# Performance work log

Hardware: AMD Instinct MI355X
Metric: run time of the kernel (lower is better)

The kernel has to match this reference:

```python
import jax, jax.numpy as jnp
import numpy as np

N = 50000          # nodes
E = 800000         # edges
F_IN, H, OUT = 512, 256, 2
BN_EPS = 1e-5


def setup_inputs() -> dict:
    key = jax.random.key(0)
    ks = jax.random.split(key, 10)
    x = jax.random.normal(ks[0], (N, F_IN), jnp.float32)
    edge_index = jax.random.randint(ks[1], (2, E), 0, N, dtype=jnp.int64)
    edge_weight = jax.random.uniform(ks[2], (E,), jnp.float32)

    def lin(k, fan_in, fan_out):
        return jax.random.normal(k, (fan_in, fan_out), jnp.float32) / np.sqrt(fan_in).astype(np.float32)

    W1, b1 = lin(ks[3], F_IN, H), jnp.zeros((H,), jnp.float32)
    W2, b2 = lin(ks[4], H, H), jnp.zeros((H,), jnp.float32)
    W3, b3 = lin(ks[5], H, OUT), jnp.zeros((OUT,), jnp.float32)
    # BatchNorm1d affine params + running stats (eval mode)
    g1, be1 = jnp.ones((H,), jnp.float32), jnp.zeros((H,), jnp.float32)
    m1 = 0.1 * jax.random.normal(ks[6], (H,), jnp.float32)
    v1 = jax.random.uniform(ks[7], (H,), jnp.float32, 0.5, 1.5)
    g2, be2 = jnp.ones((H,), jnp.float32), jnp.zeros((H,), jnp.float32)
    m2 = 0.1 * jax.random.normal(ks[8], (H,), jnp.float32)
    v2 = jax.random.uniform(ks[9], (H,), jnp.float32, 0.5, 1.5)
    return {"x": x, "edge_index": edge_index, "edge_weight": edge_weight,
            "W1": W1, "b1": b1, "g1": g1, "be1": be1, "m1": m1, "v1": v1,
            "W2": W2, "b2": b2, "g2": g2, "be2": be2, "m2": m2, "v2": v2,
            "W3": W3, "b3": b3}


def gcn_conv(x, row, col, w, W, b):
    # PyG GCNConv (eval): h = x @ W; out[col] += norm * h[row]; + b
    # row/col/w already include self-loops with weight 1.
    n = x.shape[0]
    h = x @ W                                      # [N, out]
    deg = jax.ops.segment_sum(w, col, num_segments=n)
    dinv = jnp.where(deg > 0, jax.lax.rsqrt(deg), 0.0)
    norm = dinv[row] * w * dinv[col]               # [E+N]
    out = jax.ops.segment_sum(h[row] * norm[:, None], col, num_segments=n)
    return out + b


def batchnorm_eval(x, g, be, m, v):
    return (x - m) * jax.lax.rsqrt(v + BN_EPS) * g + be


def reference(x, edge_index, edge_weight, W1, b1, g1, be1, m1, v1,
              W2, b2, g2, be2, m2, v2, W3, b3):
    n = x.shape[0]
    loops = jnp.arange(n, dtype=edge_index.dtype)
    row = jnp.concatenate([edge_index[0], loops])
    col = jnp.concatenate([edge_index[1], loops])
    w = jnp.concatenate([edge_weight, jnp.ones((n,), x.dtype)])

    h = jax.nn.relu(batchnorm_eval(gcn_conv(x, row, col, w, W1, b1), g1, be1, m1, v1))
    h = jax.nn.relu(batchnorm_eval(gcn_conv(h, row, col, w, W2, b2), g2, be2, m2, v2))
    return gcn_conv(h, row, col, w, W3, b3)
```

## Files before the change

kernel.cpp:

```cpp
#include <hip/hip_runtime.h>
#include <stdint.h>

#define F_IN 512
#define HF 256
#define OUT_F 2
#define BN_EPS 1e-5f
#define SCAN_B 256
#define LDSTR 36

typedef __attribute__((ext_vector_type(8))) short bf16x8;
typedef __attribute__((ext_vector_type(8))) unsigned short u16x8;
typedef __attribute__((ext_vector_type(4))) float f32x4;

__device__ inline float bf2f(unsigned short u) {
    union { float f; uint32_t i; } v; v.i = ((uint32_t)u) << 16; return v.f;
}
__device__ inline unsigned short f2bf(float f) {
    union { float f; uint32_t i; } v; v.f = f;
    uint32_t r = v.i + 0x7FFFu + ((v.i >> 16) & 1u);
    return (unsigned short)(r >> 16);
}

__global__ void prep_kernel(unsigned long long* __restrict__ packed,
                            const float* __restrict__ W1, unsigned short* __restrict__ W1t,
                            const float* __restrict__ W2, unsigned short* __restrict__ W2t,
                            unsigned short* __restrict__ xbf_pad,
                            unsigned short* __restrict__ bufa_pad,
                            int n, int padx, int pada) {
    int idx = blockIdx.x * blockDim.x + threadIdx.x;
    if (idx < n) { packed[idx] = 1ULL << 20; return; }
    int j = idx - n;
    if (j < F_IN * HF) {
        int nn = j >> 9, k = j & (F_IN - 1);
        W1t[j] = f2bf(W1[(size_t)k * HF + nn]);
        return;
    }
    j -= F_IN * HF;
    if (j < HF * HF) {
        int nn = j >> 8, k = j & (HF - 1);
        W2t[j] = f2bf(W2[(size_t)k * HF + nn]);
        return;
    }
    j -= HF * HF;
    if (j < padx) { xbf_pad[j] = 0; return; }
    j -= padx;
    if (j < pada) bufa_pad[j] = 0;
}

__global__ void count_conv_kernel(const int* __restrict__ col,
                                  const float* __restrict__ w,
                                  unsigned long long* __restrict__ packed,
                                  const float* __restrict__ x,
                                  unsigned short* __restrict__ xbf,
                                  int e, int nchunk) {
    int tid = blockIdx.x * blockDim.x + threadIdx.x;
    if (tid < e) {
        unsigned long long add = (1ULL << 40)
            | (unsigned long long)__float2uint_rn(w[tid] * 1048576.0f);
        atomicAdd(&packed[col[tid]], add);
    }
    const int stride = gridDim.x * blockDim.x;
    const float4* x4 = (const float4*)x;
    for (int c = tid; c < nchunk; c += stride) {
        float4 f0 = x4[2 * c];
        float4 f1 = x4[2 * c + 1];
        bf16x8 v;
        v[0] = (short)f2bf(f0.x); v[1] = (short)f2bf(f0.y);
        v[2] = (short)f2bf(f0.z); v[3] = (short)f2bf(f0.w);
        v[4] = (short)f2bf(f1.x); v[5] = (short)f2bf(f1.y);
        v[6] = (short)f2bf(f1.z); v[7] = (short)f2bf(f1.w);
        *(bf16x8*)(xbf + (size_t)c * 8) = v;
    }
}

__global__ __launch_bounds__(256)
void gemm_kernel(const unsigned short* __restrict__ A,
                 const unsigned short* __restrict__ Bt,
                 unsigned short* __restrict__ C, int K) {
    __shared__ unsigned short As[2][128 * LDSTR];
    __shared__ unsigned short Bs[2][128 * LDSTR];
    const int tid  = threadIdx.x;
    const int lane = tid & 63;
    const int wv   = tid >> 6;
    const int wrow = wv >> 1, wcol = wv & 1;
    const int m0 = blockIdx.x * 128;
    const int n0 = blockIdx.y * 128;

    const int sr = tid >> 2;
    const int sc = (tid & 3) * 8;

    const unsigned short* pa0 = A + (size_t)(m0 + sr) * K + sc;
    const unsigned short* pa1 = A + (size_t)(m0 + sr + 64) * K + sc;
    const unsigned short* pb0 = Bt + (size_t)(n0 + sr) * K + sc;
    const unsigned short* pb1 = Bt + (size_t)(n0 + sr + 64) * K + sc;

    f32x4 zero4 = {0.0f, 0.0f, 0.0f, 0.0f};
    f32x4 acc[4][4];
    #pragma unroll
    for (int i = 0; i < 4; ++i)
        #pragma unroll
        for (int j = 0; j < 4; ++j) acc[i][j] = zero4;

    const int q8 = (lane >> 4) * 8;
    const int ml = lane & 15;

    bf16x8 va0 = *(const bf16x8*)pa0;
    bf16x8 va1 = *(const bf16x8*)pa1;
    bf16x8 vb0 = *(const bf16x8*)pb0;
    bf16x8 vb1 = *(const bf16x8*)pb1;

    const int nsteps = K >> 5;
    for (int s = 0; s < nsteps; ++s) {
        const int buf = s & 1;
        *(bf16x8*)&As[buf][sr * LDSTR + sc]        = va0;
        *(bf16x8*)&As[buf][(sr + 64) * LDSTR + sc] = va1;
        *(bf16x8*)&Bs[buf][sr * LDSTR + sc]        = vb0;
        *(bf16x8*)&Bs[buf][(sr + 64) * LDSTR + sc] = vb1;
        __syncthreads();
        if (s + 1 < nsteps) {
            int off = (s + 1) * 32;
            va0 = *(const bf16x8*)(pa0 + off);
            va1 = *(const bf16x8*)(pa1 + off);
            vb0 = *(const bf16x8*)(pb0 + off);
            vb1 = *(const bf16x8*)(pb1 + off);
        }
        bf16x8 af[4], bfr[4];
        #pragma unroll
        for (int i = 0; i < 4; ++i)
            af[i] = *(const bf16x8*)&As[buf][(wrow * 64 + i * 16 + ml) * LDSTR + q8];
        #pragma unroll
        for (int j = 0; j < 4; ++j)
            bfr[j] = *(const bf16x8*)&Bs[buf][(wcol * 64 + j * 16 + ml) * LDSTR + q8];
        #pragma unroll
        for (int i = 0; i < 4; ++i)
            #pragma unroll
            for (int j = 0; j < 4; ++j)
                acc[i][j] = __builtin_amdgcn_mfma_f32_16x16x32_bf16(af[i], bfr[j], acc[i][j], 0, 0, 0);
    }

    const int q4 = (lane >> 4) * 4;
    #pragma unroll
    for (int i = 0; i < 4; ++i) {
        #pragma unroll
        for (int j = 0; j < 4; ++j) {
            #pragma unroll
            for (int rg = 0; rg < 4; ++rg) {
                int r = m0 + wrow * 64 + i * 16 + q4 + rg;
                int c = n0 + wcol * 64 + j * 16 + ml;
                C[(size_t)r * HF + c] = f2bf(acc[i][j][rg]);
            }
        }
    }
}

__global__ void scan1_kernel(const unsigned long long* __restrict__ packed,
                             int* __restrict__ local, int* __restrict__ blocksum, int n) {
    __shared__ int tmp[SCAN_B];
    int i = blockIdx.x * SCAN_B + threadIdx.x;
    int v = (i < n) ? (int)(packed[i] >> 40) : 0;
    tmp[threadIdx.x] = v;
    __syncthreads();
    for (int off = 1; off < SCAN_B; off <<= 1) {
        int t = 0;
        if ((int)threadIdx.x >= off) t = tmp[threadIdx.x - off];
        __syncthreads();
        if ((int)threadIdx.x >= off) tmp[threadIdx.x] += t;
        __syncthreads();
    }
    if (i < n) local[i] = tmp[threadIdx.x] - v;
    if (threadIdx.x == SCAN_B - 1) blocksum[blockIdx.x] = tmp[SCAN_B - 1];
}

__global__ void scan3_dinv_kernel(int* __restrict__ csr_ptr, int* __restrict__ cursor,
                                  const int* __restrict__ blocksum,
                                  const unsigned long long* __restrict__ packed,
                                  float* __restrict__ dinv, int n, int e, int nb) {
    __shared__ int red[SCAN_B];
    int t = threadIdx.x;
    red[t] = (t < nb && t < (int)blockIdx.x) ? blocksum[t] : 0;
    __syncthreads();
    for (int off = SCAN_B / 2; off > 0; off >>= 1) {
        if (t < off) red[t] += red[t + off];
        __syncthreads();
    }
    int prefix = red[0];
    int i = blockIdx.x * SCAN_B + t;
    if (i < n) {
        int val = csr_ptr[i] + prefix;
        csr_ptr[i] = val;
        cursor[i] = val;
        float deg = (float)(packed[i] & 0xFFFFFFFFFFULL) * (1.0f / 1048576.0f);
        dinv[i] = rsqrtf(deg);
    }
    if (i == 0) csr_ptr[n] = e;
}

__global__ void fill_kernel(const int* __restrict__ row, const int* __restrict__ col,
                            const float* __restrict__ w, const float* __restrict__ dinv,
                            int* __restrict__ cursor, int2* __restrict__ csr_edge, int e) {
    int i = blockIdx.x * blockDim.x + threadIdx.x;
    if (i < e) {
        int r = row[i], c = col[i];
        int pos = atomicAdd(&cursor[c], 1);
        float nrm = dinv[r] * w[i] * dinv[c];
        csr_edge[pos] = make_int2(r, __float_as_int(nrm));
    }
}

#define AGBL 8
template<int FINAL>
__global__ void agg_kernel(const unsigned short* __restrict__ h,
                           const int* __restrict__ ptr,
                           const int2* __restrict__ edge,
                           const float* __restrict__ dinv,
                           const float* __restrict__ b, const float* __restrict__ g,
                           const float* __restrict__ be, const float* __restrict__ m,
                           const float* __restrict__ v,
                           unsigned short* __restrict__ out,
                           const float* __restrict__ W3, float* __restrict__ h3, int n) {
    int wid  = (blockIdx.x * blockDim.x + threadIdx.x) >> 6;
    int lane = threadIdx.x & 63;
    if (wid >= n) return;
    const int hi = lane >> 5;
    const int l  = lane & 31;
    const int fo = l * 8;

    int p0 = ptr[wid], p1 = ptr[wid + 1];
    int deg = p1 - p0;

    float a0 = 0.f, a1 = 0.f, a2 = 0.f, a3 = 0.f;
    float a4 = 0.f, a5 = 0.f, a6 = 0.f, a7 = 0.f;

    const int nb = deg & ~15;
    for (int t = 0; t < nb; t += 16) {
        int2 ed[AGBL];
        #pragma unroll
        for (int k = 0; k < AGBL; ++k) ed[k] = edge[p0 + t + 2 * k + hi];
        u16x8 hv[AGBL];
        #pragma unroll
        for (int k = 0; k < AGBL; ++k)
            hv[k] = *(const u16x8*)(h + (size_t)(unsigned)ed[k].x * HF + fo);
        #pragma unroll
        for (int k = 0; k < AGBL; ++k) {
            float nw = __int_as_float(ed[k].y);
            a0 += nw * bf2f(hv[k][0]);
            a1 += nw * bf2f(hv[k][1]);
            a2 += nw * bf2f(hv[k][2]);
            a3 += nw * bf2f(hv[k][3]);
            a4 += nw * bf2f(hv[k][4]);
            a5 += nw * bf2f(hv[k][5]);
            a6 += nw * bf2f(hv[k][6]);
            a7 += nw * bf2f(hv[k][7]);
        }
    }
    for (int t = nb; t < deg; t += 4) {
        int2 ed[2];
        float wv2[2];
        #pragma unroll
        for (int j = 0; j < 2; ++j) {
            int idx = t + 2 * j + hi;
            int cl = idx < deg ? idx : 0;
            ed[j] = edge[p0 + cl];
            wv2[j] = (idx < deg) ? __int_as_float(ed[j].y) : 0.0f;
        }
        u16x8 hv[2];
        #pragma unroll
        for (int j = 0; j < 2; ++j)
            hv[j] = *(const u16x8*)(h + (size_t)(unsigned)ed[j].x * HF + fo);
        #pragma unroll
        for (int j = 0; j < 2; ++j) {
            float nw = wv2[j];
            a0 += nw * bf2f(hv[j][0]);
            a1 += nw * bf2f(hv[j][1]);
            a2 += nw * bf2f(hv[j][2]);
            a3 += nw * bf2f(hv[j][3]);
            a4 += nw * bf2f(hv[j][4]);
            a5 += nw * bf2f(hv[j][5]);
            a6 += nw * bf2f(hv[j][6]);
            a7 += nw * bf2f(hv[j][7]);
        }
    }

    a0 += __shfl_xor(a0, 32, 64);
    a1 += __shfl_xor(a1, 32, 64);
    a2 += __shfl_xor(a2, 32, 64);
    a3 += __shfl_xor(a3, 32, 64);
    a4 += __shfl_xor(a4, 32, 64);
    a5 += __shfl_xor(a5, 32, 64);
    a6 += __shfl_xor(a6, 32, 64);
    a7 += __shfl_xor(a7, 32, 64);

    float s = dinv[wid];
    float sl = s * s;
    u16x8 hs = *(const u16x8*)(h + (size_t)wid * HF + fo);
    a0 += sl * bf2f(hs[0]);
    a1 += sl * bf2f(hs[1]);
    a2 += sl * bf2f(hs[2]);
    a3 += sl * bf2f(hs[3]);
    a4 += sl * bf2f(hs[4]);
    a5 += sl * bf2f(hs[5]);
    a6 += sl * bf2f(hs[6]);
    a7 += sl * bf2f(hs[7]);

    float4 bb0  = *(const float4*)(b + fo),      bb1  = *(const float4*)(b + fo + 4);
    float4 gg0  = *(const float4*)(g + fo),      gg1  = *(const float4*)(g + fo + 4);
    float4 bee0 = *(const float4*)(be + fo),     bee1 = *(const float4*)(be + fo + 4);
    float4 mm0  = *(const float4*)(m + fo),      mm1  = *(const float4*)(m + fo + 4);
    float4 vv0  = *(const float4*)(v + fo),      vv1  = *(const float4*)(v + fo + 4);
    float f0 = fmaxf((a0 + bb0.x - mm0.x) * rsqrtf(vv0.x + BN_EPS) * gg0.x + bee0.x, 0.f);
    float f1 = fmaxf((a1 + bb0.y - mm0.y) * rsqrtf(vv0.y + BN_EPS) * gg0.y + bee0.y, 0.f);
    float f2 = fmaxf((a2 + bb0.z - mm0.z) * rsqrtf(vv0.z + BN_EPS) * gg0.z + bee0.z, 0.f);
    float f3 = fmaxf((a3 + bb0.w - mm0.w) * rsqrtf(vv0.w + BN_EPS) * gg0.w + bee0.w, 0.f);
    float f4 = fmaxf((a4 + bb1.x - mm1.x) * rsqrtf(vv1.x + BN_EPS) * gg1.x + bee1.x, 0.f);
    float f5 = fmaxf((a5 + bb1.y - mm1.y) * rsqrtf(vv1.y + BN_EPS) * gg1.y + bee1.y, 0.f);
    float f6 = fmaxf((a6 + bb1.z - mm1.z) * rsqrtf(vv1.z + BN_EPS) * gg1.z + bee1.z, 0.f);
    float f7 = fmaxf((a7 + bb1.w - mm1.w) * rsqrtf(vv1.w + BN_EPS) * gg1.w + bee1.w, 0.f);

    if (!FINAL) {
        if (hi == 0) {
            u16x8 o;
            o[0] = f2bf(f0); o[1] = f2bf(f1); o[2] = f2bf(f2); o[3] = f2bf(f3);
            o[4] = f2bf(f4); o[5] = f2bf(f5); o[6] = f2bf(f6); o[7] = f2bf(f7);
            *(u16x8*)(out + (size_t)wid * HF + fo) = o;
        }
    } else {
        float4 w0 = *(const float4*)(W3 + fo * 2);
        float4 w1 = *(const float4*)(W3 + fo * 2 + 4);
        float4 w2 = *(const float4*)(W3 + fo * 2 + 8);
        float4 w3 = *(const float4*)(W3 + fo * 2 + 12);
        float s0 = f0 * w0.x + f1 * w0.z + f2 * w1.x + f3 * w1.z
                 + f4 * w2.x + f5 * w2.z + f6 * w3.x + f7 * w3.z;
        float s1 = f0 * w0.y + f1 * w0.w + f2 * w1.y + f3 * w1.w
                 + f4 * w2.y + f5 * w2.w + f6 * w3.y + f7 * w3.w;
        #pragma unroll
        for (int o = 16; o > 0; o >>= 1) {
            s0 += __shfl_xor(s0, o, 64);
            s1 += __shfl_xor(s1, o, 64);
        }
        if (lane == 0) {
            h3[wid * 2 + 0] = s0;
            h3[wid * 2 + 1] = s1;
        }
    }
}

__global__ void out_kernel(const float* __restrict__ h3,
                           const int* __restrict__ ptr, const int2* __restrict__ edge,
                           const float* __restrict__ dinv,
                           const float* __restrict__ b3, float* __restrict__ out, int n) {
    int i = blockIdx.x * blockDim.x + threadIdx.x;
    if (i >= n) return;
    int p0 = ptr[i], p1 = ptr[i + 1];
    float a0 = 0.f, a1 = 0.f;
    for (int p = p0; p < p1; p += 4) {
        #pragma unroll
        for (int k = 0; k < 4; ++k) {
            int idx = p + k < p1 ? p + k : p1 - 1;
            int2 e = edge[idx];
            float nw = (p + k < p1) ? __int_as_float(e.y) : 0.0f;
            float2 u = *(const float2*)(h3 + 2 * e.x);
            a0 += nw * u.x;
            a1 += nw * u.y;
        }
    }
    float s = dinv[i];
    float sl = s * s;
    out[2 * i + 0] = a0 + sl * h3[2 * i + 0] + b3[0];
    out[2 * i + 1] = a1 + sl * h3[2 * i + 1] + b3[1];
}

static inline char* align16(char* p) {
    return (char*)(((uintptr_t)p + 15) & ~(uintptr_t)15);
}

extern "C" void kernel_launch(void* const* d_in, const int* in_sizes, int n_in,
                              void* d_out, int out_size, void* d_ws, size_t ws_size,
                              hipStream_t stream) {
    const float* x   = (const float*)d_in[0];
    const int*   ei  = (const int*)d_in[1];
    const float* ew  = (const float*)d_in[2];
    const float* W1  = (const float*)d_in[3];
    const float* b1  = (const float*)d_in[4];
    const float* g1  = (const float*)d_in[5];
    const float* be1 = (const float*)d_in[6];
    const float* m1  = (const float*)d_in[7];
    const float* v1  = (const float*)d_in[8];
    const float* W2  = (const float*)d_in[9];
    const float* b2  = (const float*)d_in[10];
    const float* g2  = (const float*)d_in[11];
    const float* be2 = (const float*)d_in[12];
    const float* m2  = (const float*)d_in[13];
    const float* v2  = (const float*)d_in[14];
    const float* W3  = (const float*)d_in[15];
    const float* b3  = (const float*)d_in[16];

    const int N  = in_sizes[0] / F_IN;
    const int E  = in_sizes[2];
    const int MP = (N + 127) & ~127;
    const int* row = ei;
    const int* col = ei + E;

    char* wsb = (char*)d_ws;
    unsigned long long* packed = (unsigned long long*)wsb; wsb = align16(wsb + (size_t)N * 8);
    float* dinv     = (float*)wsb;          wsb = align16(wsb + (size_t)N * 4);
    int*   csr_ptr  = (int*)wsb;            wsb = align16(wsb + (size_t)(N + 1) * 4);
    int*   cursor   = (int*)wsb;            wsb = align16(wsb + (size_t)N * 4);
    int*   blocksum = (int*)wsb;            wsb = align16(wsb + (size_t)SCAN_B * 4);
    int2*  csr_edge = (int2*)wsb;           wsb = align16(wsb + (size_t)E * 8);
    unsigned short* W1t = (unsigned short*)wsb;  wsb = align16(wsb + (size_t)F_IN * HF * 2);
    unsigned short* W2t = (unsigned short*)wsb;  wsb = align16(wsb + (size_t)HF * HF * 2);
    unsigned short* xbf  = (unsigned short*)wsb; wsb = align16(wsb + (size_t)MP * F_IN * 2);
    unsigned short* bufh = (unsigned short*)wsb; wsb = align16(wsb + (size_t)MP * HF * 2);
    unsigned short* bufa = (unsigned short*)wsb; wsb = align16(wsb + (size_t)MP * HF * 2);
    float* h3 = (float*)wsb;                wsb = align16(wsb + (size_t)N * OUT_F * 4);
    float* outf = (float*)d_out;

    const int TB = 256;
    const int nscan = (N + SCAN_B - 1) / SCAN_B;
    const int padx = (MP - N) * F_IN;
    const int pada = (MP - N) * HF;
    const int preptot = N + F_IN * HF + HF * HF + padx + pada;
    const int ncc = (E + TB - 1) / TB;
    const int nchunk = (N * F_IN) / 8;

    prep_kernel<<<(preptot + TB - 1) / TB, TB, 0, stream>>>(
        packed, W1, W1t, W2, W2t, xbf + (size_t)N * F_IN, bufa + (size_t)N * HF, N, padx, pada);

    count_conv_kernel<<<ncc, TB, 0, stream>>>(col, ew, packed, x, xbf, E, nchunk);

    scan1_kernel<<<nscan, SCAN_B, 0, stream>>>(packed, csr_ptr, blocksum, N);
    scan3_dinv_kernel<<<nscan, SCAN_B, 0, stream>>>(csr_ptr, cursor, blocksum, packed, dinv, N, E, nscan);
    fill_kernel<<<(E + TB - 1) / TB, TB, 0, stream>>>(row, col, ew, dinv, cursor, csr_edge, E);

    dim3 ggrid(MP / 128, HF / 128);

    gemm_kernel<<<ggrid, TB, 0, stream>>>(xbf, W1t, bufh, F_IN);
    agg_kernel<0><<<((size_t)N * 64 + TB - 1) / TB, TB, 0, stream>>>(
        bufh, csr_ptr, csr_edge, dinv, b1, g1, be1, m1, v1, bufa, nullptr, nullptr, N);

    gemm_kernel<<<ggrid, TB, 0, stream>>>(bufa, W2t, bufh, HF);
    agg_kernel<1><<<((size_t)N * 64 + TB - 1) / TB, TB, 0, stream>>>(
        bufh, csr_ptr, csr_edge, dinv, b2, g2, be2, m2, v2, nullptr, W3, h3, N);

    out_kernel<<<(N + TB - 1) / TB, TB, 0, stream>>>(h3, csr_ptr, csr_edge, dinv, b3, outf, N);
}
```

Baseline: 467.1 us.

## Fuse fp32-to-bf16 input conversion into first GEMM and prefetch edges in aggregation

The first GEMM now reads the fp32 node features directly and converts them to bf16 while loading its A tile, clamping out-of-range rows instead of relying on a zero-padded bf16 copy. This drops the separate conversion pass that wrote a bf16 copy of x, along with its workspace and padding fill. Because the GEMM grid has two column blocks, each fp32 row is read twice and converted twice, so the GEMM does more memory traffic and ALU work. Separately, the aggregation kernel's main loop prefetches the next batch of CSR edge entries before accumulating the current one, to hide the latency of the dependent gather.

```diff
diff --git a/kernel.cpp b/kernel.cpp
--- a/kernel.cpp
+++ b/kernel.cpp
@@ -24,9 +24,8 @@
 __global__ void prep_kernel(unsigned long long* __restrict__ packed,
                             const float* __restrict__ W1, unsigned short* __restrict__ W1t,
                             const float* __restrict__ W2, unsigned short* __restrict__ W2t,
-                            unsigned short* __restrict__ xbf_pad,
                             unsigned short* __restrict__ bufa_pad,
-                            int n, int padx, int pada) {
+                            int n, int pada) {
     int idx = blockIdx.x * blockDim.x + threadIdx.x;
     if (idx < n) { packed[idx] = 1ULL << 20; return; }
     int j = idx - n;
@@ -42,41 +41,42 @@
         return;
     }
     j -= HF * HF;
-    if (j < padx) { xbf_pad[j] = 0; return; }
-    j -= padx;
     if (j < pada) bufa_pad[j] = 0;
 }
 
-__global__ void count_conv_kernel(const int* __restrict__ col,
-                                  const float* __restrict__ w,
-                                  unsigned long long* __restrict__ packed,
-                                  const float* __restrict__ x,
-                                  unsigned short* __restrict__ xbf,
-                                  int e, int nchunk) {
+__global__ void count_kernel(const int* __restrict__ col,
+                             const float* __restrict__ w,
+                             unsigned long long* __restrict__ packed, int e) {
     int tid = blockIdx.x * blockDim.x + threadIdx.x;
     if (tid < e) {
         unsigned long long add = (1ULL << 40)
             | (unsigned long long)__float2uint_rn(w[tid] * 1048576.0f);
         atomicAdd(&packed[col[tid]], add);
     }
-    const int stride = gridDim.x * blockDim.x;
-    const float4* x4 = (const float4*)x;
-    for (int c = tid; c < nchunk; c += stride) {
-        float4 f0 = x4[2 * c];
-        float4 f1 = x4[2 * c + 1];
-        bf16x8 v;
-        v[0] = (short)f2bf(f0.x); v[1] = (short)f2bf(f0.y);
-        v[2] = (short)f2bf(f0.z); v[3] = (short)f2bf(f0.w);
-        v[4] = (short)f2bf(f1.x); v[5] = (short)f2bf(f1.y);
-        v[6] = (short)f2bf(f1.z); v[7] = (short)f2bf(f1.w);
-        *(bf16x8*)(xbf + (size_t)c * 8) = v;
-    }
-}
-
+}
+
+template<int AFP32>
+__device__ inline bf16x8 load_a(const void* base, size_t elem_off) {
+    if constexpr (AFP32) {
+        const float* p = (const float*)base + elem_off;
+        float4 f0 = *(const float4*)p;
+        float4 f1 = *(const float4*)(p + 4);
+        bf16x8 r;
+        r[0] = (short)f2bf(f0.x); r[1] = (short)f2bf(f0.y);
+        r[2] = (short)f2bf(f0.z); r[3] = (short)f2bf(f0.w);
+        r[4] = (short)f2bf(f1.x); r[5] = (short)f2bf(f1.y);
+        r[6] = (short)f2bf(f1.z); r[7] = (short)f2bf(f1.w);
+        return r;
+    } else {
+        return *(const bf16x8*)((const unsigned short*)base + elem_off);
+    }
+}
+
+template<int AFP32>
 __global__ __launch_bounds__(256)
-void gemm_kernel(const unsigned short* __restrict__ A,
+void gemm_kernel(const void* __restrict__ Av,
                  const unsigned short* __restrict__ Bt,
-                 unsigned short* __restrict__ C, int K) {
+                 unsigned short* __restrict__ C, int K, int rowclamp) {
     __shared__ unsigned short As[2][128 * LDSTR];
     __shared__ unsigned short Bs[2][128 * LDSTR];
     const int tid  = threadIdx.x;
@@ -89,8 +89,14 @@
     const int sr = tid >> 2;
     const int sc = (tid & 3) * 8;
 
-    const unsigned short* pa0 = A + (size_t)(m0 + sr) * K + sc;
-    const unsigned short* pa1 = A + (size_t)(m0 + sr + 64) * K + sc;
+    int ra0 = m0 + sr, ra1 = m0 + sr + 64;
+    if (AFP32) {
+        ra0 = ra0 < rowclamp ? ra0 : rowclamp - 1;
+        ra1 = ra1 < rowclamp ? ra1 : rowclamp - 1;
+    }
+    const size_t offA0 = (size_t)ra0 * K + sc;
+    const size_t offA1 = (size_t)ra1 * K + sc;
+
     const unsigned short* pb0 = Bt + (size_t)(n0 + sr) * K + sc;
     const unsigned short* pb1 = Bt + (size_t)(n0 + sr + 64) * K + sc;
 
@@ -104,8 +110,8 @@
     const int q8 = (lane >> 4) * 8;
     const int ml = lane & 15;
 
-    bf16x8 va0 = *(const bf16x8*)pa0;
-    bf16x8 va1 = *(const bf16x8*)pa1;
+    bf16x8 va0 = load_a<AFP32>(Av, offA0);
+    bf16x8 va1 = load_a<AFP32>(Av, offA1);
     bf16x8 vb0 = *(const bf16x8*)pb0;
     bf16x8 vb1 = *(const bf16x8*)pb1;
 
@@ -119,8 +125,8 @@
         __syncthreads();
         if (s + 1 < nsteps) {
             int off = (s + 1) * 32;
-            va0 = *(const bf16x8*)(pa0 + off);
-            va1 = *(const bf16x8*)(pa1 + off);
+            va0 = load_a<AFP32>(Av, offA0 + off);
+            va1 = load_a<AFP32>(Av, offA1 + off);
             vb0 = *(const bf16x8*)(pb0 + off);
             vb1 = *(const bf16x8*)(pb1 + off);
         }
@@ -232,25 +238,33 @@
     float a4 = 0.f, a5 = 0.f, a6 = 0.f, a7 = 0.f;
 
     const int nb = deg & ~15;
-    for (int t = 0; t < nb; t += 16) {
-        int2 ed[AGBL];
-        #pragma unroll
-        for (int k = 0; k < AGBL; ++k) ed[k] = edge[p0 + t + 2 * k + hi];
-        u16x8 hv[AGBL];
-        #pragma unroll
-        for (int k = 0; k < AGBL; ++k)
-            hv[k] = *(const u16x8*)(h + (size_t)(unsigned)ed[k].x * HF + fo);
-        #pragma unroll
-        for (int k = 0; k < AGBL; ++k) {
-            float nw = __int_as_float(ed[k].y);
-            a0 += nw * bf2f(hv[k][0]);
-            a1 += nw * bf2f(hv[k][1]);
-            a2 += nw * bf2f(hv[k][2]);
-            a3 += nw * bf2f(hv[k][3]);
-            a4 += nw * bf2f(hv[k][4]);
-            a5 += nw * bf2f(hv[k][5]);
-            a6 += nw * bf2f(hv[k][6]);
-            a7 += nw * bf2f(hv[k][7]);
+    if (nb > 0) {
+        int2 edc[AGBL];
+        #pragma unroll
+        for (int k = 0; k < AGBL; ++k) edc[k] = edge[p0 + 2 * k + hi];
+        for (int t = 0; t < nb; t += 16) {
+            u16x8 hv[AGBL];
+            #pragma unroll
+            for (int k = 0; k < AGBL; ++k)
+                hv[k] = *(const u16x8*)(h + (size_t)(unsigned)edc[k].x * HF + fo);
+            float wv[AGBL];
+            #pragma unroll
+            for (int k = 0; k < AGBL; ++k) wv[k] = __int_as_float(edc[k].y);
+            if (t + 16 < nb) {
+                #pragma unroll
+                for (int k = 0; k < AGBL; ++k) edc[k] = edge[p0 + t + 16 + 2 * k + hi];
+            }
+            #pragma unroll
+            for (int k = 0; k < AGBL; ++k) {
+                a0 += wv[k] * bf2f(hv[k][0]);
+                a1 += wv[k] * bf2f(hv[k][1]);
+                a2 += wv[k] * bf2f(hv[k][2]);
+                a3 += wv[k] * bf2f(hv[k][3]);
+                a4 += wv[k] * bf2f(hv[k][4]);
+                a5 += wv[k] * bf2f(hv[k][5]);
+                a6 += wv[k] * bf2f(hv[k][6]);
+                a7 += wv[k] * bf2f(hv[k][7]);
+            }
         }
     }
     for (int t = nb; t < deg; t += 4) {
@@ -409,7 +423,6 @@
     int2*  csr_edge = (int2*)wsb;           wsb = align16(wsb + (size_t)E * 8);
     unsigned short* W1t = (unsigned short*)wsb;  wsb = align16(wsb + (size_t)F_IN * HF * 2);
     unsigned short* W2t = (unsigned short*)wsb;  wsb = align16(wsb + (size_t)HF * HF * 2);
-    unsigned short* xbf  = (unsigned short*)wsb; wsb = align16(wsb + (size_t)MP * F_IN * 2);
     unsigned short* bufh = (unsigned short*)wsb; wsb = align16(wsb + (size_t)MP * HF * 2);
     unsigned short* bufa = (unsigned short*)wsb; wsb = align16(wsb + (size_t)MP * HF * 2);
     float* h3 = (float*)wsb;                wsb = align16(wsb + (size_t)N * OUT_F * 4);
@@ -417,16 +430,13 @@
 
     const int TB = 256;
     const int nscan = (N + SCAN_B - 1) / SCAN_B;
-    const int padx = (MP - N) * F_IN;
     const int pada = (MP - N) * HF;
-    const int preptot = N + F_IN * HF + HF * HF + padx + pada;
-    const int ncc = (E + TB - 1) / TB;
-    const int nchunk = (N * F_IN) / 8;
+    const int preptot = N + F_IN * HF + HF * HF + pada;
 
     prep_kernel<<<(preptot + TB - 1) / TB, TB, 0, stream>>>(
-        packed, W1, W1t, W2, W2t, xbf + (size_t)N * F_IN, bufa + (size_t)N * HF, N, padx, pada);
-
-    count_conv_kernel<<<ncc, TB, 0, stream>>>(col, ew, packed, x, xbf, E, nchunk);
+        packed, W1, W1t, W2, W2t, bufa + (size_t)N * HF, N, pada);
+
+    count_kernel<<<(E + TB - 1) / TB, TB, 0, stream>>>(col, ew, packed, E);
 
     scan1_kernel<<<nscan, SCAN_B, 0, stream>>>(packed, csr_ptr, blocksum, N);
     scan3_dinv_kernel<<<nscan, SCAN_B, 0, stream>>>(csr_ptr, cursor, blocksum, packed, dinv, N, E, nscan);
@@ -434,11 +444,11 @@
 
     dim3 ggrid(MP / 128, HF / 128);
 
-    gemm_kernel<<<ggrid, TB, 0, stream>>>(xbf, W1t, bufh, F_IN);
+    gemm_kernel<1><<<ggrid, TB, 0, stream>>>(x, W1t, bufh, F_IN, N);
     agg_kernel<0><<<((size_t)N * 64 + TB - 1) / TB, TB, 0, stream>>>(
         bufh, csr_ptr, csr_edge, dinv, b1, g1, be1, m1, v1, bufa, nullptr, nullptr, N);
 
-    gemm_kernel<<<ggrid, TB, 0, stream>>>(bufa, W2t, bufh, HF);
+    gemm_kernel<0><<<ggrid, TB, 0, stream>>>(bufa, W2t, bufh, HF, MP);
     agg_kernel<1><<<((size_t)N * 64 + TB - 1) / TB, TB, 0, stream>>>(
         bufh, csr_ptr, csr_edge, dinv, b2, g2, be2, m2, v2, nullptr, W3, h3, N);
 
```

Measured after the change: 476.6 us. +2.0%, slower.

## Fuse graph setup kernels into one persistent kernel with grid barriers

Applied to the files above, without the earlier changes.

Merges the prep, count/convert, two scan and fill kernels into a single persistent setup kernel of 768 blocks that separates phases with a software grid-wide barrier built on atomics. This removes four kernel launches and the gaps between them in the preprocessing pipeline. It adds a memset of the barrier counters, relies on all 768 blocks being co-resident (launch bounds 256,4 on 256 CUs) to avoid deadlock, and the atomic spin barriers cost time of their own.

```diff
diff --git a/kernel.cpp b/kernel.cpp
--- a/kernel.cpp
+++ b/kernel.cpp
@@ -7,6 +7,7 @@
 #define BN_EPS 1e-5f
 #define SCAN_B 256
 #define LDSTR 36
+#define NBSETUP 768
 
 typedef __attribute__((ext_vector_type(8))) short bf16x8;
 typedef __attribute__((ext_vector_type(8))) unsigned short u16x8;
@@ -21,47 +22,56 @@
     return (unsigned short)(r >> 16);
 }
 
-__global__ void prep_kernel(unsigned long long* __restrict__ packed,
-                            const float* __restrict__ W1, unsigned short* __restrict__ W1t,
-                            const float* __restrict__ W2, unsigned short* __restrict__ W2t,
-                            unsigned short* __restrict__ xbf_pad,
-                            unsigned short* __restrict__ bufa_pad,
-                            int n, int padx, int pada) {
-    int idx = blockIdx.x * blockDim.x + threadIdx.x;
-    if (idx < n) { packed[idx] = 1ULL << 20; return; }
-    int j = idx - n;
-    if (j < F_IN * HF) {
+__device__ inline void grid_sync(int* cnt, int* gen, int nb) {
+    __syncthreads();
+    if (threadIdx.x == 0) {
+        __threadfence();
+        int g = __hip_atomic_load(gen, __ATOMIC_RELAXED, __HIP_MEMORY_SCOPE_AGENT);
+        if (__hip_atomic_fetch_add(cnt, 1, __ATOMIC_ACQ_REL, __HIP_MEMORY_SCOPE_AGENT) == nb - 1) {
+            __hip_atomic_store(cnt, 0, __ATOMIC_RELAXED, __HIP_MEMORY_SCOPE_AGENT);
+            __hip_atomic_store(gen, g + 1, __ATOMIC_RELEASE, __HIP_MEMORY_SCOPE_AGENT);
+        } else {
+            while (__hip_atomic_load(gen, __ATOMIC_ACQUIRE, __HIP_MEMORY_SCOPE_AGENT) == g)
+                __builtin_amdgcn_s_sleep(2);
+        }
+        __threadfence();
+    }
+    __syncthreads();
+}
+
+__global__ __launch_bounds__(256, 4)
+void setup_kernel(unsigned long long* __restrict__ packed,
+                  const float* __restrict__ W1, unsigned short* __restrict__ W1t,
+                  const float* __restrict__ W2, unsigned short* __restrict__ W2t,
+                  unsigned short* __restrict__ xbf,
+                  unsigned short* __restrict__ bufa,
+                  const float* __restrict__ x,
+                  const int* __restrict__ row, const int* __restrict__ col,
+                  const float* __restrict__ ew,
+                  int* __restrict__ csr_ptr, int* __restrict__ cursor,
+                  int* __restrict__ blocksum, float* __restrict__ dinv,
+                  int2* __restrict__ csr_edge,
+                  int* __restrict__ bar,
+                  int n, int e, int padx, int pada, int nscan, int nchunk) {
+    __shared__ int tmp[SCAN_B];
+    const int gsz  = gridDim.x * blockDim.x;
+    const int gtid = blockIdx.x * blockDim.x + threadIdx.x;
+    int* cnt = bar;
+    int* gen = bar + 1;
+
+    for (int i = gtid; i < n; i += gsz) packed[i] = 1ULL << 20;
+    for (int j = gtid; j < F_IN * HF; j += gsz) {
         int nn = j >> 9, k = j & (F_IN - 1);
         W1t[j] = f2bf(W1[(size_t)k * HF + nn]);
-        return;
-    }
-    j -= F_IN * HF;
-    if (j < HF * HF) {
+    }
+    for (int j = gtid; j < HF * HF; j += gsz) {
         int nn = j >> 8, k = j & (HF - 1);
         W2t[j] = f2bf(W2[(size_t)k * HF + nn]);
-        return;
-    }
-    j -= HF * HF;
-    if (j < padx) { xbf_pad[j] = 0; return; }
-    j -= padx;
-    if (j < pada) bufa_pad[j] = 0;
-}
-
-__global__ void count_conv_kernel(const int* __restrict__ col,
-                                  const float* __restrict__ w,
-                                  unsigned long long* __restrict__ packed,
-                                  const float* __restrict__ x,
-                                  unsigned short* __restrict__ xbf,
-                                  int e, int nchunk) {
-    int tid = blockIdx.x * blockDim.x + threadIdx.x;
-    if (tid < e) {
-        unsigned long long add = (1ULL << 40)
-            | (unsigned long long)__float2uint_rn(w[tid] * 1048576.0f);
-        atomicAdd(&packed[col[tid]], add);
-    }
-    const int stride = gridDim.x * blockDim.x;
+    }
+    for (int j = gtid; j < padx; j += gsz) xbf[(size_t)n * F_IN + j] = 0;
+    for (int j = gtid; j < pada; j += gsz) bufa[(size_t)n * HF + j] = 0;
     const float4* x4 = (const float4*)x;
-    for (int c = tid; c < nchunk; c += stride) {
+    for (int c = gtid; c < nchunk; c += gsz) {
         float4 f0 = x4[2 * c];
         float4 f1 = x4[2 * c + 1];
         bf16x8 v;
@@ -70,6 +80,59 @@
         v[4] = (short)f2bf(f1.x); v[5] = (short)f2bf(f1.y);
         v[6] = (short)f2bf(f1.z); v[7] = (short)f2bf(f1.w);
         *(bf16x8*)(xbf + (size_t)c * 8) = v;
+    }
+    grid_sync(cnt, gen, (int)gridDim.x);
+
+    for (int i = gtid; i < e; i += gsz) {
+        unsigned long long add = (1ULL << 40)
+            | (unsigned long long)__float2uint_rn(ew[i] * 1048576.0f);
+        atomicAdd(&packed[col[i]], add);
+    }
+    grid_sync(cnt, gen, (int)gridDim.x);
+
+    if ((int)blockIdx.x < nscan) {
+        int i = blockIdx.x * SCAN_B + threadIdx.x;
+        int v = (i < n) ? (int)(packed[i] >> 40) : 0;
+        tmp[threadIdx.x] = v;
+        __syncthreads();
+        for (int off = 1; off < SCAN_B; off <<= 1) {
+            int t = 0;
+            if ((int)threadIdx.x >= off) t = tmp[threadIdx.x - off];
+            __syncthreads();
+            if ((int)threadIdx.x >= off) tmp[threadIdx.x] += t;
+            __syncthreads();
+        }
+        if (i < n) csr_ptr[i] = tmp[threadIdx.x] - v;
+        if (threadIdx.x == SCAN_B - 1) blocksum[blockIdx.x] = tmp[SCAN_B - 1];
+    }
+    grid_sync(cnt, gen, (int)gridDim.x);
+
+    if ((int)blockIdx.x < nscan) {
+        int t = threadIdx.x;
+        tmp[t] = (t < nscan && t < (int)blockIdx.x) ? blocksum[t] : 0;
+        __syncthreads();
+        for (int off = SCAN_B / 2; off > 0; off >>= 1) {
+            if (t < off) tmp[t] += tmp[t + off];
+            __syncthreads();
+        }
+        int prefix = tmp[0];
+        int i = blockIdx.x * SCAN_B + t;
+        if (i < n) {
+            int val = csr_ptr[i] + prefix;
+            csr_ptr[i] = val;
+            cursor[i] = val;
+            float deg = (float)(packed[i] & 0xFFFFFFFFFFULL) * (1.0f / 1048576.0f);
+            dinv[i] = rsqrtf(deg);
+        }
+        if (i == 0) csr_ptr[n] = e;
+    }
+    grid_sync(cnt, gen, (int)gridDim.x);
+
+    for (int i = gtid; i < e; i += gsz) {
+        int r = row[i], c = col[i];
+        int pos = atomicAdd(&cursor[c], 1);
+        float nrm = dinv[r] * ew[i] * dinv[c];
+        csr_edge[pos] = make_int2(r, __float_as_int(nrm));
     }
 }
 
@@ -150,60 +213,6 @@
                 C[(size_t)r * HF + c] = f2bf(acc[i][j][rg]);
             }
         }
-    }
-}
-
-__global__ void scan1_kernel(const unsigned long long* __restrict__ packed,
-                             int* __restrict__ local, int* __restrict__ blocksum, int n) {
-    __shared__ int tmp[SCAN_B];
-    int i = blockIdx.x * SCAN_B + threadIdx.x;
-    int v = (i < n) ? (int)(packed[i] >> 40) : 0;
-    tmp[threadIdx.x] = v;
-    __syncthreads();
-    for (int off = 1; off < SCAN_B; off <<= 1) {
-        int t = 0;
-        if ((int)threadIdx.x >= off) t = tmp[threadIdx.x - off];
-        __syncthreads();
-        if ((int)threadIdx.x >= off) tmp[threadIdx.x] += t;
-        __syncthreads();
-    }
-    if (i < n) local[i] = tmp[threadIdx.x] - v;
-    if (threadIdx.x == SCAN_B - 1) blocksum[blockIdx.x] = tmp[SCAN_B - 1];
-}
-
-__global__ void scan3_dinv_kernel(int* __restrict__ csr_ptr, int* __restrict__ cursor,
-                                  const int* __restrict__ blocksum,
-                                  const unsigned long long* __restrict__ packed,
-                                  float* __restrict__ dinv, int n, int e, int nb) {
-    __shared__ int red[SCAN_B];
-    int t = threadIdx.x;
-    red[t] = (t < nb && t < (int)blockIdx.x) ? blocksum[t] : 0;
-    __syncthreads();
-    for (int off = SCAN_B / 2; off > 0; off >>= 1) {
-        if (t < off) red[t] += red[t + off];
-        __syncthreads();
-    }
-    int prefix = red[0];
-    int i = blockIdx.x * SCAN_B + t;
-    if (i < n) {
-        int val = csr_ptr[i] + prefix;
-        csr_ptr[i] = val;
-        cursor[i] = val;
-        float deg = (float)(packed[i] & 0xFFFFFFFFFFULL) * (1.0f / 1048576.0f);
-        dinv[i] = rsqrtf(deg);
-    }
-    if (i == 0) csr_ptr[n] = e;
-}
-
-__global__ void fill_kernel(const int* __restrict__ row, const int* __restrict__ col,
-                            const float* __restrict__ w, const float* __restrict__ dinv,
-                            int* __restrict__ cursor, int2* __restrict__ csr_edge, int e) {
-    int i = blockIdx.x * blockDim.x + threadIdx.x;
-    if (i < e) {
-        int r = row[i], c = col[i];
-        int pos = atomicAdd(&cursor[c], 1);
-        float nrm = dinv[r] * w[i] * dinv[c];
-        csr_edge[pos] = make_int2(r, __float_as_int(nrm));
     }
 }
 
@@ -413,24 +422,21 @@
     unsigned short* bufh = (unsigned short*)wsb; wsb = align16(wsb + (size_t)MP * HF * 2);
     unsigned short* bufa = (unsigned short*)wsb; wsb = align16(wsb + (size_t)MP * HF * 2);
     float* h3 = (float*)wsb;                wsb = align16(wsb + (size_t)N * OUT_F * 4);
+    int*   bar = (int*)wsb;                 wsb = align16(wsb + 2 * 4);
     float* outf = (float*)d_out;
 
     const int TB = 256;
     const int nscan = (N + SCAN_B - 1) / SCAN_B;
     const int padx = (MP - N) * F_IN;
     const int pada = (MP - N) * HF;
-    const int preptot = N + F_IN * HF + HF * HF + padx + pada;
-    const int ncc = (E + TB - 1) / TB;
     const int nchunk = (N * F_IN) / 8;
 
-    prep_kernel<<<(preptot + TB - 1) / TB, TB, 0, stream>>>(
-        packed, W1, W1t, W2, W2t, xbf + (size_t)N * F_IN, bufa + (size_t)N * HF, N, padx, pada);
-
-    count_conv_kernel<<<ncc, TB, 0, stream>>>(col, ew, packed, x, xbf, E, nchunk);
-
-    scan1_kernel<<<nscan, SCAN_B, 0, stream>>>(packed, csr_ptr, blocksum, N);
-    scan3_dinv_kernel<<<nscan, SCAN_B, 0, stream>>>(csr_ptr, cursor, blocksum, packed, dinv, N, E, nscan);
-    fill_kernel<<<(E + TB - 1) / TB, TB, 0, stream>>>(row, col, ew, dinv, cursor, csr_edge, E);
+    (void)hipMemsetAsync(bar, 0, 2 * sizeof(int), stream);
+
+    setup_kernel<<<NBSETUP, TB, 0, stream>>>(
+        packed, W1, W1t, W2, W2t, xbf, bufa, x, row, col, ew,
+        csr_ptr, cursor, blocksum, dinv, csr_edge, bar,
+        N, E, padx, pada, nscan, nchunk);
 
     dim3 ggrid(MP / 128, HF / 128);
 
```

Result: slower. 922.3 us (+97.4%).

## Fuse prep kernels, co-launch CSR fill with first GEMM, add XCD swizzle

Applied to the files above, without the earlier changes.

Merges weight transpose, padding zeroing, degree counting and x-to-bf16 conversion into one grid-stride front kernel, and replaces the packed-init with a memset plus adding the self-loop degree in scan3. The CSR fill blocks are appended to the first GEMM launch so the atomic scatter overlaps with MFMA work. GEMM blocks are remapped with an XCD-aware swizzle so neighbouring tiles land on the same chiplet for L2 reuse. Together these cut launch count and idle tails, at the cost of heterogeneous blocks sharing LDS allocation and a fixed 1024-block front grid.

```diff
diff --git a/kernel.cpp b/kernel.cpp
--- a/kernel.cpp
+++ b/kernel.cpp
@@ -21,47 +21,33 @@
     return (unsigned short)(r >> 16);
 }
 
-__global__ void prep_kernel(unsigned long long* __restrict__ packed,
-                            const float* __restrict__ W1, unsigned short* __restrict__ W1t,
-                            const float* __restrict__ W2, unsigned short* __restrict__ W2t,
-                            unsigned short* __restrict__ xbf_pad,
-                            unsigned short* __restrict__ bufa_pad,
-                            int n, int padx, int pada) {
-    int idx = blockIdx.x * blockDim.x + threadIdx.x;
-    if (idx < n) { packed[idx] = 1ULL << 20; return; }
-    int j = idx - n;
-    if (j < F_IN * HF) {
+__global__ void front_kernel(unsigned long long* __restrict__ packed,
+                             const float* __restrict__ W1, unsigned short* __restrict__ W1t,
+                             const float* __restrict__ W2, unsigned short* __restrict__ W2t,
+                             const float* __restrict__ x, unsigned short* __restrict__ xbf,
+                             unsigned short* __restrict__ bufa_pad,
+                             const int* __restrict__ col, const float* __restrict__ ew,
+                             int n, int e, int padx, int pada, int nchunk) {
+    const int gsz  = gridDim.x * blockDim.x;
+    const int gtid = blockIdx.x * blockDim.x + threadIdx.x;
+
+    for (int i = gtid; i < e; i += gsz) {
+        unsigned long long add = (1ULL << 40)
+            | (unsigned long long)__float2uint_rn(ew[i] * 1048576.0f);
+        atomicAdd(&packed[col[i]], add);
+    }
+    for (int j = gtid; j < F_IN * HF; j += gsz) {
         int nn = j >> 9, k = j & (F_IN - 1);
         W1t[j] = f2bf(W1[(size_t)k * HF + nn]);
-        return;
-    }
-    j -= F_IN * HF;
-    if (j < HF * HF) {
+    }
+    for (int j = gtid; j < HF * HF; j += gsz) {
         int nn = j >> 8, k = j & (HF - 1);
         W2t[j] = f2bf(W2[(size_t)k * HF + nn]);
-        return;
-    }
-    j -= HF * HF;
-    if (j < padx) { xbf_pad[j] = 0; return; }
-    j -= padx;
-    if (j < pada) bufa_pad[j] = 0;
-}
-
-__global__ void count_conv_kernel(const int* __restrict__ col,
-                                  const float* __restrict__ w,
-                                  unsigned long long* __restrict__ packed,
-                                  const float* __restrict__ x,
-                                  unsigned short* __restrict__ xbf,
-                                  int e, int nchunk) {
-    int tid = blockIdx.x * blockDim.x + threadIdx.x;
-    if (tid < e) {
-        unsigned long long add = (1ULL << 40)
-            | (unsigned long long)__float2uint_rn(w[tid] * 1048576.0f);
-        atomicAdd(&packed[col[tid]], add);
-    }
-    const int stride = gridDim.x * blockDim.x;
+    }
+    for (int j = gtid; j < padx; j += gsz) xbf[(size_t)n * F_IN + j] = 0;
+    for (int j = gtid; j < pada; j += gsz) bufa_pad[j] = 0;
     const float4* x4 = (const float4*)x;
-    for (int c = tid; c < nchunk; c += stride) {
+    for (int c = gtid; c < nchunk; c += gsz) {
         float4 f0 = x4[2 * c];
         float4 f1 = x4[2 * c + 1];
         bf16x8 v;
@@ -73,18 +59,64 @@
     }
 }
 
-__global__ __launch_bounds__(256)
-void gemm_kernel(const unsigned short* __restrict__ A,
-                 const unsigned short* __restrict__ Bt,
-                 unsigned short* __restrict__ C, int K) {
-    __shared__ unsigned short As[2][128 * LDSTR];
-    __shared__ unsigned short Bs[2][128 * LDSTR];
+__global__ void scan1_kernel(const unsigned long long* __restrict__ packed,
+                             int* __restrict__ local, int* __restrict__ blocksum, int n) {
+    __shared__ int tmp[SCAN_B];
+    int i = blockIdx.x * SCAN_B + threadIdx.x;
+    int v = (i < n) ? (int)(packed[i] >> 40) : 0;
+    tmp[threadIdx.x] = v;
+    __syncthreads();
+    for (int off = 1; off < SCAN_B; off <<= 1) {
+        int t = 0;
+        if ((int)threadIdx.x >= off) t = tmp[threadIdx.x - off];
+        __syncthreads();
+        if ((int)threadIdx.x >= off) tmp[threadIdx.x] += t;
+        __syncthreads();
+    }
+    if (i < n) local[i] = tmp[threadIdx.x] - v;
+    if (threadIdx.x == SCAN_B - 1) blocksum[blockIdx.x] = tmp[SCAN_B - 1];
+}
+
+__global__ void scan3_dinv_kernel(int* __restrict__ csr_ptr, int* __restrict__ cursor,
+                                  const int* __restrict__ blocksum,
+                                  const unsigned long long* __restrict__ packed,
+                                  float* __restrict__ dinv, int n, int e, int nb) {
+    __shared__ int red[SCAN_B];
+    int t = threadIdx.x;
+    red[t] = (t < nb && t < (int)blockIdx.x) ? blocksum[t] : 0;
+    __syncthreads();
+    for (int off = SCAN_B / 2; off > 0; off >>= 1) {
+        if (t < off) red[t] += red[t + off];
+        __syncthreads();
+    }
+    int prefix = red[0];
+    int i = blockIdx.x * SCAN_B + t;
+    if (i < n) {
+        int val = csr_ptr[i] + prefix;
+        csr_ptr[i] = val;
+        cursor[i] = val;
+        float deg = (float)((packed[i] & 0xFFFFFFFFFFULL) + (1ULL << 20)) * (1.0f / 1048576.0f);
+        dinv[i] = rsqrtf(deg);
+    }
+    if (i == 0) csr_ptr[n] = e;
+}
+
+__device__ inline int xcd_swizzle(int orig, int ngemm) {
+    int xcd = orig & 7, j = orig >> 3;
+    int q = ngemm >> 3, r8 = ngemm & 7;
+    return (xcd < r8 ? xcd * (q + 1) : r8 * (q + 1) + (xcd - r8) * q) + j;
+}
+
+__device__ inline void gemm_body(const unsigned short* __restrict__ A,
+                                 const unsigned short* __restrict__ Bt,
+                                 unsigned short* __restrict__ C, int K,
+                                 int m0, int n0,
+                                 unsigned short (*As)[128 * LDSTR],
+                                 unsigned short (*Bs)[128 * LDSTR]) {
     const int tid  = threadIdx.x;
     const int lane = tid & 63;
     const int wv   = tid >> 6;
     const int wrow = wv >> 1, wcol = wv & 1;
-    const int m0 = blockIdx.x * 128;
-    const int n0 = blockIdx.y * 128;
 
     const int sr = tid >> 2;
     const int sc = (tid & 3) * 8;
@@ -153,58 +185,37 @@
     }
 }
 
-__global__ void scan1_kernel(const unsigned long long* __restrict__ packed,
-                             int* __restrict__ local, int* __restrict__ blocksum, int n) {
-    __shared__ int tmp[SCAN_B];
-    int i = blockIdx.x * SCAN_B + threadIdx.x;
-    int v = (i < n) ? (int)(packed[i] >> 40) : 0;
-    tmp[threadIdx.x] = v;
-    __syncthreads();
-    for (int off = 1; off < SCAN_B; off <<= 1) {
-        int t = 0;
-        if ((int)threadIdx.x >= off) t = tmp[threadIdx.x - off];
-        __syncthreads();
-        if ((int)threadIdx.x >= off) tmp[threadIdx.x] += t;
-        __syncthreads();
-    }
-    if (i < n) local[i] = tmp[threadIdx.x] - v;
-    if (threadIdx.x == SCAN_B - 1) blocksum[blockIdx.x] = tmp[SCAN_B - 1];
-}
-
-__global__ void scan3_dinv_kernel(int* __restrict__ csr_ptr, int* __restrict__ cursor,
-                                  const int* __restrict__ blocksum,
-                                  const unsigned long long* __restrict__ packed,
-                                  float* __restrict__ dinv, int n, int e, int nb) {
-    __shared__ int red[SCAN_B];
-    int t = threadIdx.x;
-    red[t] = (t < nb && t < (int)blockIdx.x) ? blocksum[t] : 0;
-    __syncthreads();
-    for (int off = SCAN_B / 2; off > 0; off >>= 1) {
-        if (t < off) red[t] += red[t + off];
-        __syncthreads();
-    }
-    int prefix = red[0];
-    int i = blockIdx.x * SCAN_B + t;
-    if (i < n) {
-        int val = csr_ptr[i] + prefix;
-        csr_ptr[i] = val;
-        cursor[i] = val;
-        float deg = (float)(packed[i] & 0xFFFFFFFFFFULL) * (1.0f / 1048576.0f);
-        dinv[i] = rsqrtf(deg);
-    }
-    if (i == 0) csr_ptr[n] = e;
-}
-
-__global__ void fill_kernel(const int* __restrict__ row, const int* __restrict__ col,
-                            const float* __restrict__ w, const float* __restrict__ dinv,
-                            int* __restrict__ cursor, int2* __restrict__ csr_edge, int e) {
-    int i = blockIdx.x * blockDim.x + threadIdx.x;
-    if (i < e) {
-        int r = row[i], c = col[i];
-        int pos = atomicAdd(&cursor[c], 1);
-        float nrm = dinv[r] * w[i] * dinv[c];
-        csr_edge[pos] = make_int2(r, __float_as_int(nrm));
-    }
+__global__ __launch_bounds__(256)
+void fillgemm_kernel(const unsigned short* __restrict__ A,
+                     const unsigned short* __restrict__ Bt,
+                     unsigned short* __restrict__ C, int K, int ngemm,
+                     const int* __restrict__ row, const int* __restrict__ col,
+                     const float* __restrict__ w, const float* __restrict__ dinv,
+                     int* __restrict__ cursor, int2* __restrict__ csr_edge, int e) {
+    __shared__ unsigned short As[2][128 * LDSTR];
+    __shared__ unsigned short Bs[2][128 * LDSTR];
+    if ((int)blockIdx.x >= ngemm) {
+        int i = ((int)blockIdx.x - ngemm) * blockDim.x + threadIdx.x;
+        if (i < e) {
+            int r = row[i], c = col[i];
+            int pos = atomicAdd(&cursor[c], 1);
+            float nrm = dinv[r] * w[i] * dinv[c];
+            csr_edge[pos] = make_int2(r, __float_as_int(nrm));
+        }
+        return;
+    }
+    int logical = xcd_swizzle(blockIdx.x, ngemm);
+    gemm_body(A, Bt, C, K, (logical >> 1) * 128, (logical & 1) * 128, As, Bs);
+}
+
+__global__ __launch_bounds__(256)
+void gemm_kernel(const unsigned short* __restrict__ A,
+                 const unsigned short* __restrict__ Bt,
+                 unsigned short* __restrict__ C, int K, int ngemm) {
+    __shared__ unsigned short As[2][128 * LDSTR];
+    __shared__ unsigned short Bs[2][128 * LDSTR];
+    int logical = xcd_swizzle(blockIdx.x, ngemm);
+    gemm_body(A, Bt, C, K, (logical >> 1) * 128, (logical & 1) * 128, As, Bs);
 }
 
 #define AGBL 8
@@ -419,26 +430,26 @@
     const int nscan = (N + SCAN_B - 1) / SCAN_B;
     const int padx = (MP - N) * F_IN;
     const int pada = (MP - N) * HF;
-    const int preptot = N + F_IN * HF + HF * HF + padx + pada;
-    const int ncc = (E + TB - 1) / TB;
     const int nchunk = (N * F_IN) / 8;
-
-    prep_kernel<<<(preptot + TB - 1) / TB, TB, 0, stream>>>(
-        packed, W1, W1t, W2, W2t, xbf + (size_t)N * F_IN, bufa + (size_t)N * HF, N, padx, pada);
-
-    count_conv_kernel<<<ncc, TB, 0, stream>>>(col, ew, packed, x, xbf, E, nchunk);
+    const int ngemm = (MP / 128) * 2;
+    const int nfill = (E + TB - 1) / TB;
+
+    (void)hipMemsetAsync(packed, 0, (size_t)N * 8, stream);
+
+    front_kernel<<<1024, TB, 0, stream>>>(
+        packed, W1, W1t, W2, W2t, x, xbf, bufa + (size_t)N * HF,
+        col, ew, N, E, padx, pada, nchunk);
 
     scan1_kernel<<<nscan, SCAN_B, 0, stream>>>(packed, csr_ptr, blocksum, N);
     scan3_dinv_kernel<<<nscan, SCAN_B, 0, stream>>>(csr_ptr, cursor, blocksum, packed, dinv, N, E, nscan);
-    fill_kernel<<<(E + TB - 1) / TB, TB, 0, stream>>>(row, col, ew, dinv, cursor, csr_edge, E);
-
-    dim3 ggrid(MP / 128, HF / 128);
-
-    gemm_kernel<<<ggrid, TB, 0, stream>>>(xbf, W1t, bufh, F_IN);
+
+    fillgemm_kernel<<<ngemm + nfill, TB, 0, stream>>>(
+        xbf, W1t, bufh, F_IN, ngemm, row, col, ew, dinv, cursor, csr_edge, E);
+
     agg_kernel<0><<<((size_t)N * 64 + TB - 1) / TB, TB, 0, stream>>>(
         bufh, csr_ptr, csr_edge, dinv, b1, g1, be1, m1, v1, bufa, nullptr, nullptr, N);
 
-    gemm_kernel<<<ggrid, TB, 0, stream>>>(bufa, W2t, bufh, HF);
+    gemm_kernel<<<ngemm, TB, 0, stream>>>(bufa, W2t, bufh, HF, ngemm);
     agg_kernel<1><<<((size_t)N * 64 + TB - 1) / TB, TB, 0, stream>>>(
         bufh, csr_ptr, csr_edge, dinv, b2, g2, be2, m2, v2, nullptr, W3, h3, N);
 
```

After: 518.2 us. 1.11x slower.
